# Kernel optimization log

Hardware: AMD Instinct MI355X
Metric: run time of the kernel (lower is better)

## Reference

```python
import jax, jax.numpy as jnp
import numpy as np


def setup_inputs() -> dict:
    key = jax.random.key(0)
    # batch of 1D signals; DST is applied along the last dimension
    x = jax.random.normal(key, (16384, 1024), dtype=jnp.float32)
    return {"x": x}


def reference(x):
    # DST-II: y_k = sum_{n=0}^{N-1} x_n * sin(pi/N * (n + 1/2) * (k + 1))
    # (The original docstring says 'cos' but the op is a discrete SINE transform;
    #  the DREAMPlace kernel computes the DST-II above via FFT-style tricks.)
    N = x.shape[-1]
    n = jnp.arange(N, dtype=x.dtype)
    k = jnp.arange(N, dtype=x.dtype)
    # [N, N] sine basis: rows indexed by n (input), cols by k (output)
    S = jnp.sin((jnp.pi / N) * (n[:, None] + 0.5) * (k[None, :] + 1.0))
    # batched transform over leading dims
    lead = x.shape[:-1]
    y = jnp.einsum('bn,nk->bk', x.reshape(-1, N), S)
    return y.reshape(*lead, N)
```

## Files before the change

### kernel.cpp

```cpp
#include <hip/hip_runtime.h>
#include <cstdint>


__device__ __forceinline__ float sinr(float r) {
  return __builtin_amdgcn_sinf(r);
}
__device__ __forceinline__ float cosr(float r) {
  float t = r + 0.25f;
  t -= (t >= 1.0f) ? 1.0f : 0.0f;
  return __builtin_amdgcn_sinf(t);
}

__global__ __launch_bounds__(256) void dst_fft(const float* __restrict__ X,
                                               float* __restrict__ Y) {
  static constexpr int BR4[16] = {0, 8, 4, 12, 2, 10, 6, 14,
                                  1, 9, 5, 13, 3, 11, 7, 15};
  static constexpr float W16C[8] = {1.0f, 0.9238795325f, 0.7071067812f,
                                    0.3826834324f, 0.0f, -0.3826834324f,
                                    -0.7071067812f, -0.9238795325f};
  static constexpr float W16S[8] = {-0.0f, -0.3826834324f, -0.7071067812f,
                                    -0.9238795325f, -1.0f, -0.9238795325f,
                                    -0.7071067812f, -0.3826834324f};

  __shared__ __align__(16) float lds_all[4][64 * 32];

  const int t = threadIdx.x;
  const int l = t & 63;
  const int w = t >> 6;
  float* lds = &lds_all[w][0];
  const int wid = blockIdx.x * 4 + w;

  const int c = l & 3;
  const int m2l = l >> 2;
  const int e = ((c & 1) << 1) | (c >> 1);
  const int sstar = BR4[m2l];
  const int chb = sstar >> 1;
  const int subo = (sstar & 1) * 2;

  float gc[16], gs[16];
#pragma unroll
  for (int i = 0; i < 16; ++i) {
    float r = (float)(l * BR4[i]) * (1.0f / 1024.0f);
    gc[i] = cosr(r);
    gs[i] = -sinr(r);
  }

#pragma unroll
  for (int it = 0; it < 2; ++it) {
    const int row = wid * 2 + it;
    const float* xr = X + (size_t)row * 1024;

    float re[16], im[16], odd[8];
#pragma unroll
    for (int j = 0; j < 8; ++j) {
      float2 v = *(const float2*)(xr + 2 * l + 128 * j);
      re[j] = v.x;
      odd[j] = v.y;
    }
#pragma unroll
    for (int j = 0; j < 8; ++j)
      re[15 - j] = -__shfl_xor(odd[j], 63);
#pragma unroll
    for (int i = 0; i < 16; ++i) im[i] = 0.0f;

#pragma unroll
    for (int H = 8; H >= 1; H >>= 1) {
#pragma unroll
      for (int b = 0; b < 16; b += 2 * H) {
#pragma unroll
        for (int o = 0; o < H; ++o) {
          int i0 = b + o, i1 = i0 + H;
          float ar = re[i0] - re[i1], ai = im[i0] - im[i1];
          re[i0] += re[i1];
          im[i0] += im[i1];
          int tw = o * (8 / H);
          re[i1] = ar * W16C[tw] - ai * W16S[tw];
          im[i1] = ar * W16S[tw] + ai * W16C[tw];
        }
      }
    }
#pragma unroll
    for (int i = 0; i < 16; ++i) {
      float tr = re[i] * gc[i] - im[i] * gs[i];
      im[i] = re[i] * gs[i] + im[i] * gc[i];
      re[i] = tr;
    }

    __asm__ volatile("s_waitcnt lgkmcnt(0)" ::: "memory");
#pragma unroll
    for (int ch = 0; ch < 8; ++ch) {
      float4 v = make_float4(re[2 * ch], im[2 * ch],
                             re[2 * ch + 1], im[2 * ch + 1]);
      *(float4*)(lds + l * 32 + ((ch ^ (l & 7)) * 4)) = v;
    }
    __asm__ volatile("s_waitcnt lgkmcnt(0)" ::: "memory");
#pragma unroll
    for (int i = 0; i < 16; ++i) {
      int r = c + 4 * BR4[i];
      int cp = chb ^ (r & 7);
      float2 v = *(const float2*)(lds + r * 32 + cp * 4 + subo);
      re[i] = v.x;
      im[i] = v.y;
    }

#pragma unroll
    for (int H = 1; H <= 8; H <<= 1) {
#pragma unroll
      for (int b = 0; b < 16; b += 2 * H) {
#pragma unroll
        for (int o = 0; o < H; ++o) {
          int i0 = b + o, i1 = i0 + H;
          int tw = o * (8 / H);
          float tr = re[i1] * W16C[tw] - im[i1] * W16S[tw];
          float ti = re[i1] * W16S[tw] + im[i1] * W16C[tw];
          re[i1] = re[i0] - tr;
          im[i1] = im[i0] - ti;
          re[i0] += tr;
          im[i0] += ti;
        }
      }
    }

#pragma unroll
    for (int m = 0; m < 16; ++m) {
      float r = (float)(c * m) * (1.0f / 64.0f);
      float tc = cosr(r), ts = -sinr(r);
      float tr = re[m] * tc - im[m] * ts;
      im[m] = re[m] * ts + im[m] * tc;
      re[m] = tr;
    }

    {
      const float sgA = (c & 2) ? -1.0f : 1.0f;
      const bool rot = (c == 3);
      const float sgB = (c & 1) ? -1.0f : 1.0f;
#pragma unroll
      for (int i = 0; i < 16; ++i) {
        float tr = __shfl_xor(re[i], 2), ti = __shfl_xor(im[i], 2);
        float ar = tr + sgA * re[i], ai = ti + sgA * im[i];
        float br = rot ? ai : ar;
        float bi = rot ? -ar : ai;
        tr = __shfl_xor(br, 1);
        ti = __shfl_xor(bi, 1);
        re[i] = tr + sgB * br;
        im[i] = ti + sgB * bi;
      }
    }

    float* yr = Y + (size_t)row * 1024 + (1023 - m2l - 256 * e);
#pragma unroll
    for (int s2 = 0; s2 < 16; ++s2) {
      int j = m2l + 16 * s2 + 256 * e;
      float r = (float)j * (1.0f / 4096.0f);
      yr[-16 * s2] = re[s2] * cosr(r) + im[s2] * sinr(r);
    }
  }
}

extern "C" void kernel_launch(void* const* d_in, const int* in_sizes, int n_in,
                              void* d_out, int out_size, void* d_ws, size_t ws_size,
                              hipStream_t stream) {
  const float* X = (const float*)d_in[0];
  float* Y = (float*)d_out;
  dst_fft<<<dim3(2048), dim3(256), 0, stream>>>(X, Y);
}
```

Before: 119.9 us.

## Process one row per wave, halve LDS via two-pass transpose, specialize trivial twiddles

After: 161.7 us. +34.8%, slower.

```diff
diff --git a/kernel.cpp b/kernel.cpp
--- a/kernel.cpp
+++ b/kernel.cpp
@@ -1,6 +1,15 @@
 #include <hip/hip_runtime.h>
 #include <cstdint>
 
+
+static constexpr int BR4[16] = {0, 8, 4, 12, 2, 10, 6, 14,
+                                1, 9, 5, 13, 3, 11, 7, 15};
+static constexpr float W16C[8] = {1.0f, 0.9238795325f, 0.7071067812f,
+                                  0.3826834324f, 0.0f, -0.3826834324f,
+                                  -0.7071067812f, -0.9238795325f};
+static constexpr float W16S[8] = {-0.0f, -0.3826834324f, -0.7071067812f,
+                                  -0.9238795325f, -1.0f, -0.9238795325f,
+                                  -0.7071067812f, -0.3826834324f};
 
 __device__ __forceinline__ float sinr(float r) {
   return __builtin_amdgcn_sinf(r);
@@ -11,149 +20,166 @@
   return __builtin_amdgcn_sinf(t);
 }
 
-__global__ __launch_bounds__(256) void dst_fft(const float* __restrict__ X,
-                                               float* __restrict__ Y) {
-  static constexpr int BR4[16] = {0, 8, 4, 12, 2, 10, 6, 14,
-                                  1, 9, 5, 13, 3, 11, 7, 15};
-  static constexpr float W16C[8] = {1.0f, 0.9238795325f, 0.7071067812f,
-                                    0.3826834324f, 0.0f, -0.3826834324f,
-                                    -0.7071067812f, -0.9238795325f};
-  static constexpr float W16S[8] = {-0.0f, -0.3826834324f, -0.7071067812f,
-                                    -0.9238795325f, -1.0f, -0.9238795325f,
-                                    -0.7071067812f, -0.3826834324f};
+__device__ __forceinline__ void twmul(int tw, float xr, float xi,
+                                      float& yr, float& yi) {
+  if (tw == 0) {
+    yr = xr; yi = xi;
+  } else if (tw == 4) {
+    yr = xi; yi = -xr;
+  } else if (tw == 2) {
+    yr = 0.70710678118f * (xr + xi);
+    yi = 0.70710678118f * (xi - xr);
+  } else if (tw == 6) {
+    yr = 0.70710678118f * (xi - xr);
+    yi = -0.70710678118f * (xr + xi);
+  } else {
+    yr = xr * W16C[tw] - xi * W16S[tw];
+    yi = xr * W16S[tw] + xi * W16C[tw];
+  }
+}
 
-  __shared__ __align__(16) float lds_all[4][64 * 32];
+__global__ __launch_bounds__(256, 8) void dst_fft(const float* __restrict__ X,
+                                                  float* __restrict__ Y) {
+  __shared__ __align__(16) float lds_all[4][64 * 16];
 
   const int t = threadIdx.x;
   const int l = t & 63;
   const int w = t >> 6;
   float* lds = &lds_all[w][0];
-  const int wid = blockIdx.x * 4 + w;
+  const int row = blockIdx.x * 4 + w;
 
   const int c = l & 3;
   const int m2l = l >> 2;
   const int e = ((c & 1) << 1) | (c >> 1);
-  const int sstar = BR4[m2l];
-  const int chb = sstar >> 1;
+  const int sstar = (int)(__brev((unsigned)m2l) >> 28);
+  const int pl = sstar >> 3;
+  const int ccs = (sstar >> 1) & 3;
   const int subo = (sstar & 1) * 2;
 
-  float gc[16], gs[16];
+  const float* xr = X + (size_t)row * 1024;
+
+  float re[16], im[16], odd[8];
 #pragma unroll
-  for (int i = 0; i < 16; ++i) {
-    float r = (float)(l * BR4[i]) * (1.0f / 1024.0f);
-    gc[i] = cosr(r);
-    gs[i] = -sinr(r);
+  for (int j = 0; j < 8; ++j) {
+    float2 v = *(const float2*)(xr + 2 * l + 128 * j);
+    re[j] = v.x;
+    odd[j] = v.y;
+  }
+#pragma unroll
+  for (int j = 0; j < 8; ++j)
+    re[15 - j] = -__shfl_xor(odd[j], 63);
+
+#pragma unroll
+  for (int o = 0; o < 8; ++o) {
+    float d = re[o] - re[o + 8];
+    re[o] += re[o + 8];
+    im[o] = 0.0f;
+    if (o == 0) {
+      re[8] = d;            im[8] = 0.0f;
+    } else if (o == 4) {
+      re[12] = 0.0f;        im[12] = -d;
+    } else {
+      re[o + 8] = d * W16C[o];
+      im[o + 8] = d * W16S[o];
+    }
+  }
+#pragma unroll
+  for (int H = 4; H >= 1; H >>= 1) {
+#pragma unroll
+    for (int b = 0; b < 16; b += 2 * H) {
+#pragma unroll
+      for (int o = 0; o < H; ++o) {
+        int i0 = b + o, i1 = i0 + H;
+        float ar = re[i0] - re[i1], ai = im[i0] - im[i1];
+        re[i0] += re[i1];
+        im[i0] += im[i1];
+        twmul(o * (8 / H), ar, ai, re[i1], im[i1]);
+      }
+    }
   }
 
 #pragma unroll
-  for (int it = 0; it < 2; ++it) {
-    const int row = wid * 2 + it;
-    const float* xr = X + (size_t)row * 1024;
+  for (int i = 1; i < 16; ++i) {
+    float r = (float)(l * BR4[i]) * (1.0f / 1024.0f);
+    float tc = cosr(r), ts = -sinr(r);
+    float tr = re[i] * tc - im[i] * ts;
+    im[i] = re[i] * ts + im[i] * tc;
+    re[i] = tr;
+  }
 
-    float re[16], im[16], odd[8];
+  float re2[16], im2[16];
 #pragma unroll
-    for (int j = 0; j < 8; ++j) {
-      float2 v = *(const float2*)(xr + 2 * l + 128 * j);
-      re[j] = v.x;
-      odd[j] = v.y;
+  for (int p = 0; p < 2; ++p) {
+    __asm__ volatile("s_waitcnt lgkmcnt(0)" ::: "memory");
+#pragma unroll
+    for (int cc = 0; cc < 4; ++cc) {
+      int ch = 4 * p + cc;
+      float4 v = make_float4(re[2 * ch], im[2 * ch],
+                             re[2 * ch + 1], im[2 * ch + 1]);
+      *(float4*)(lds + l * 16 + ((cc ^ ((l >> 1) & 3)) & 3) * 4) = v;
     }
+    __asm__ volatile("s_waitcnt lgkmcnt(0)" ::: "memory");
+    if (pl == p) {
 #pragma unroll
-    for (int j = 0; j < 8; ++j)
-      re[15 - j] = -__shfl_xor(odd[j], 63);
-#pragma unroll
-    for (int i = 0; i < 16; ++i) im[i] = 0.0f;
+      for (int i = 0; i < 16; ++i) {
+        int r = c + 4 * BR4[i];
+        int q = (ccs ^ ((r >> 1) & 3)) & 3;
+        float2 v = *(const float2*)(lds + r * 16 + q * 4 + subo);
+        re2[i] = v.x;
+        im2[i] = v.y;
+      }
+    }
+  }
 
 #pragma unroll
-    for (int H = 8; H >= 1; H >>= 1) {
+  for (int H = 1; H <= 8; H <<= 1) {
 #pragma unroll
-      for (int b = 0; b < 16; b += 2 * H) {
+    for (int b = 0; b < 16; b += 2 * H) {
 #pragma unroll
-        for (int o = 0; o < H; ++o) {
-          int i0 = b + o, i1 = i0 + H;
-          float ar = re[i0] - re[i1], ai = im[i0] - im[i1];
-          re[i0] += re[i1];
-          im[i0] += im[i1];
-          int tw = o * (8 / H);
-          re[i1] = ar * W16C[tw] - ai * W16S[tw];
-          im[i1] = ar * W16S[tw] + ai * W16C[tw];
-        }
+      for (int o = 0; o < H; ++o) {
+        int i0 = b + o, i1 = i0 + H;
+        float tr, ti;
+        twmul(o * (8 / H), re2[i1], im2[i1], tr, ti);
+        re2[i1] = re2[i0] - tr;
+        im2[i1] = im2[i0] - ti;
+        re2[i0] += tr;
+        im2[i0] += ti;
       }
     }
+  }
+
+#pragma unroll
+  for (int m = 1; m < 16; ++m) {
+    float r = (float)(c * m) * (1.0f / 64.0f);
+    float tc = cosr(r), ts = -sinr(r);
+    float tr = re2[m] * tc - im2[m] * ts;
+    im2[m] = re2[m] * ts + im2[m] * tc;
+    re2[m] = tr;
+  }
+
+  {
+    const float sgA = (c & 2) ? -1.0f : 1.0f;
+    const bool rot = (c == 3);
+    const float sgB = (c & 1) ? -1.0f : 1.0f;
 #pragma unroll
     for (int i = 0; i < 16; ++i) {
-      float tr = re[i] * gc[i] - im[i] * gs[i];
-      im[i] = re[i] * gs[i] + im[i] * gc[i];
-      re[i] = tr;
+      float tr = __shfl_xor(re2[i], 2), ti = __shfl_xor(im2[i], 2);
+      float ar = tr + sgA * re2[i], ai = ti + sgA * im2[i];
+      float br = rot ? ai : ar;
+      float bi = rot ? -ar : ai;
+      tr = __shfl_xor(br, 1);
+      ti = __shfl_xor(bi, 1);
+      re2[i] = tr + sgB * br;
+      im2[i] = ti + sgB * bi;
     }
+  }
 
-    __asm__ volatile("s_waitcnt lgkmcnt(0)" ::: "memory");
+  float* yr = Y + (size_t)row * 1024 + (1023 - m2l - 256 * e);
 #pragma unroll
-    for (int ch = 0; ch < 8; ++ch) {
-      float4 v = make_float4(re[2 * ch], im[2 * ch],
-                             re[2 * ch + 1], im[2 * ch + 1]);
-      *(float4*)(lds + l * 32 + ((ch ^ (l & 7)) * 4)) = v;
-    }
-    __asm__ volatile("s_waitcnt lgkmcnt(0)" ::: "memory");
-#pragma unroll
-    for (int i = 0; i < 16; ++i) {
-      int r = c + 4 * BR4[i];
-      int cp = chb ^ (r & 7);
-      float2 v = *(const float2*)(lds + r * 32 + cp * 4 + subo);
-      re[i] = v.x;
-      im[i] = v.y;
-    }
-
-#pragma unroll
-    for (int H = 1; H <= 8; H <<= 1) {
-#pragma unroll
-      for (int b = 0; b < 16; b += 2 * H) {
-#pragma unroll
-        for (int o = 0; o < H; ++o) {
-          int i0 = b + o, i1 = i0 + H;
-          int tw = o * (8 / H);
-          float tr = re[i1] * W16C[tw] - im[i1] * W16S[tw];
-          float ti = re[i1] * W16S[tw] + im[i1] * W16C[tw];
-          re[i1] = re[i0] - tr;
-          im[i1] = im[i0] - ti;
-          re[i0] += tr;
-          im[i0] += ti;
-        }
-      }
-    }
-
-#pragma unroll
-    for (int m = 0; m < 16; ++m) {
-      float r = (float)(c * m) * (1.0f / 64.0f);
-      float tc = cosr(r), ts = -sinr(r);
-      float tr = re[m] * tc - im[m] * ts;
-      im[m] = re[m] * ts + im[m] * tc;
-      re[m] = tr;
-    }
-
-    {
-      const float sgA = (c & 2) ? -1.0f : 1.0f;
-      const bool rot = (c == 3);
-      const float sgB = (c & 1) ? -1.0f : 1.0f;
-#pragma unroll
-      for (int i = 0; i < 16; ++i) {
-        float tr = __shfl_xor(re[i], 2), ti = __shfl_xor(im[i], 2);
-        float ar = tr + sgA * re[i], ai = ti + sgA * im[i];
-        float br = rot ? ai : ar;
-        float bi = rot ? -ar : ai;
-        tr = __shfl_xor(br, 1);
-        ti = __shfl_xor(bi, 1);
-        re[i] = tr + sgB * br;
-        im[i] = ti + sgB * bi;
-      }
-    }
-
-    float* yr = Y + (size_t)row * 1024 + (1023 - m2l - 256 * e);
-#pragma unroll
-    for (int s2 = 0; s2 < 16; ++s2) {
-      int j = m2l + 16 * s2 + 256 * e;
-      float r = (float)j * (1.0f / 4096.0f);
-      yr[-16 * s2] = re[s2] * cosr(r) + im[s2] * sinr(r);
-    }
+  for (int s2 = 0; s2 < 16; ++s2) {
+    int j = m2l + 16 * s2 + 256 * e;
+    float r = (float)j * (1.0f / 4096.0f);
+    yr[-16 * s2] = re2[s2] * cosr(r) + im2[s2] * sinr(r);
   }
 }
 
@@ -162,5 +188,5 @@
                               hipStream_t stream) {
   const float* X = (const float*)d_in[0];
   float* Y = (float*)d_out;
-  dst_fft<<<dim3(2048), dim3(256), 0, stream>>>(X, Y);
+  dst_fft<<<dim3(4096), dim3(256), 0, stream>>>(X, Y);
 }
```
